# Performance work log

Measured on AMD Instinct MI355X. Metric: run time of the kernel, lower is better.

The kernel has to match this reference:

```python
import jax, jax.numpy as jnp
import numpy as np

N_NODES = 50000
N_EDGES = 640000
IN_CH = 128
OUT_CH = 128


def setup_inputs() -> dict:
    key = jax.random.key(0)
    k1, k2, k3, k4 = jax.random.split(key, 4)
    x = jax.random.normal(k1, (N_NODES, IN_CH), dtype=jnp.float32)
    edge_index = jax.random.randint(k2, (2, N_EDGES), 0, N_NODES, dtype=jnp.int32)
    # nn.Linear params: W [out, in], b [out]
    bound = 1.0 / np.sqrt(IN_CH)
    W = jax.random.uniform(k3, (OUT_CH, IN_CH), minval=-bound, maxval=bound, dtype=jnp.float32)
    b = jax.random.uniform(k4, (OUT_CH,), minval=-bound, maxval=bound, dtype=jnp.float32)
    return {"x": x, "edge_index": edge_index, "W": W, "b": b}


def reference(x, edge_index, W, b):
    row, col = edge_index[0], edge_index[1]
    num_nodes = x.shape[0]
    # degree of each destination node (clamped to >= 1)
    deg = jax.ops.segment_sum(jnp.ones(row.shape[0], dtype=x.dtype), row,
                              num_segments=num_nodes)
    deg = jnp.maximum(deg, 1.0)
    # gather neighbor features and scatter-add into destinations
    agg = jax.ops.segment_sum(x[col], row, num_segments=num_nodes)
    agg = agg / deg[:, None]
    # residual + linear
    return (x + agg) @ W.T + b
```

## Files before the change

kernel.cpp:

```cpp
#include <hip/hip_runtime.h>

#define N_NODES 50000
#define N_EDGES 640000
#define CH 128
#define NBINS 391
#define BINCAP 2048
#define CAPR 48
#define NTILES 3125
#define FILLB 157

typedef __bf16 bf16_t;
typedef bf16_t bf16x8 __attribute__((ext_vector_type(8)));
typedef float f32x4 __attribute__((ext_vector_type(4)));

__device__ __forceinline__ ushort f2bf(float f) {
  union { float f; unsigned u; } v; v.f = f;
  unsigned r = v.u + 0x7FFFu + ((v.u >> 16) & 1u);
  return (ushort)(r >> 16);
}
__device__ __forceinline__ float bflo(unsigned u) {
  union { unsigned u; float f; } v; v.u = u << 16; return v.f;
}
__device__ __forceinline__ float bfhi(unsigned u) {
  union { unsigned u; float f; } v; v.u = u & 0xFFFF0000u; return v.f;
}
__device__ __forceinline__ unsigned pack2(float lo, float hi) {
  return (unsigned)f2bf(lo) | ((unsigned)f2bf(hi) << 16);
}


__global__ __launch_bounds__(256) void fill_conv(const int* __restrict__ row,
                                                 const int* __restrict__ col,
                                                 int* __restrict__ bincur,
                                                 unsigned* __restrict__ binArr,
                                                 const float4* __restrict__ x4,
                                                 uint4* __restrict__ xb4,
                                                 const float4* __restrict__ W4,
                                                 uint4* __restrict__ Wb4) {
  int bid = blockIdx.x;
  int tid = threadIdx.x;
  if (bid < FILLB) {
    __shared__ int lh[NBINS];
    __shared__ int gb[NBINS];
    for (int i = tid; i < NBINS; i += 256) lh[i] = 0;
    __syncthreads();
    int base = bid * 4096 + tid * 16;
    bool act = base < N_EDGES;
    int rr[16], cc[16], bi[16], rk[16];
    if (act) {
#pragma unroll
      for (int u = 0; u < 4; ++u) {
        int4 r4 = *(const int4*)(row + base + u * 4);
        int4 c4 = *(const int4*)(col + base + u * 4);
        rr[u * 4 + 0] = r4.x; rr[u * 4 + 1] = r4.y; rr[u * 4 + 2] = r4.z; rr[u * 4 + 3] = r4.w;
        cc[u * 4 + 0] = c4.x; cc[u * 4 + 1] = c4.y; cc[u * 4 + 2] = c4.z; cc[u * 4 + 3] = c4.w;
      }
#pragma unroll
      for (int i = 0; i < 16; ++i) {
        bi[i] = rr[i] >> 7;
        rk[i] = atomicAdd(&lh[bi[i]], 1);
      }
    }
    __syncthreads();
    for (int i = tid; i < NBINS; i += 256) {
      int c = lh[i];
      gb[i] = c ? atomicAdd(&bincur[i], c) : 0;
    }
    __syncthreads();
    if (act) {
#pragma unroll
      for (int i = 0; i < 16; ++i) {
        int pos = gb[bi[i]] + rk[i];
        if (pos < BINCAP) {
          binArr[bi[i] * BINCAP + pos] =
              ((unsigned)(rr[i] & 127) << 16) | (unsigned)cc[i];
        }
      }
    }
  } else if (bid < FILLB + 3125) {
    int i = (bid - FILLB) * 256 + tid;
    float4 a = x4[i * 2], b = x4[i * 2 + 1];
    uint4 o;
    o.x = pack2(a.x, a.y); o.y = pack2(a.z, a.w);
    o.z = pack2(b.x, b.y); o.w = pack2(b.z, b.w);
    xb4[i] = o;
  } else {
    for (int i = tid; i < 2048; i += 256) {
      float4 c = W4[i * 2], d = W4[i * 2 + 1];
      uint4 w;
      w.x = pack2(c.x, c.y); w.y = pack2(c.z, c.w);
      w.z = pack2(d.x, d.y); w.w = pack2(d.z, d.w);
      Wb4[i] = w;
    }
  }
}

__global__ __launch_bounds__(128) void fused(const uint4* __restrict__ xb4,
                                             const int* __restrict__ bincnt,
                                             const uint4* __restrict__ binArr4,
                                             const uint4* __restrict__ Wb4,
                                             const float4* __restrict__ bias4,
                                             float4* __restrict__ out4) {
  __shared__ ushort hT[16 * CH];
  __shared__ ushort colL[16 * CAPR];
  __shared__ int rowcnt[16];
  int tid = threadIdx.x;
  int g = blockIdx.x;
  int m0 = g * 16;

  if (tid < 16) rowcnt[tid] = 0;
  __syncthreads();
  {
    int b = g >> 3;
    int sub = g & 7;
    int bc = bincnt[b]; bc = bc < BINCAP ? bc : BINCAP;
    const uint4* seg4 = binArr4 + b * (BINCAP / 4);
    for (int j = tid; j * 4 < bc; j += 128) {
      uint4 rv = seg4[j];
      int base = j * 4;
      unsigned recs[4] = {rv.x, rv.y, rv.z, rv.w};
#pragma unroll
      for (int i = 0; i < 4; ++i) {
        unsigned rec = recs[i];
        if (base + i < bc && (int)((rec >> 20) & 7) == sub) {
          int lr = (rec >> 16) & 15;
          int p = atomicAdd(&rowcnt[lr], 1);
          if (p < CAPR) colL[lr * CAPR + p] = (ushort)(rec & 0xFFFFu);
        }
      }
    }
  }
  __syncthreads();

  int wv = tid >> 6;
  int lane = tid & 63;
  int q = lane & 15;
  int grp = lane >> 4;
#pragma unroll
  for (int t = 0; t < 2; ++t) {
    int r = wv * 8 + t * 4 + grp;
    int node = m0 + r;
    int deg = rowcnt[r];
    int degc = deg < CAPR ? deg : CAPR;
    const ushort* arow = colL + r * CAPR;
    float acc[8] = {0.f, 0.f, 0.f, 0.f, 0.f, 0.f, 0.f, 0.f};
    int e = 0;
    for (; e + 3 < degc; e += 4) {
      uint2 ids = *(const uint2*)(arow + e);
      int n0 = ids.x & 0xFFFF, n1 = ids.x >> 16;
      int n2 = ids.y & 0xFFFF, n3 = ids.y >> 16;
      uint4 v0 = xb4[n0 * 16 + q];
      uint4 v1 = xb4[n1 * 16 + q];
      uint4 v2 = xb4[n2 * 16 + q];
      uint4 v3 = xb4[n3 * 16 + q];
      acc[0] += bflo(v0.x); acc[1] += bfhi(v0.x); acc[2] += bflo(v0.y); acc[3] += bfhi(v0.y);
      acc[4] += bflo(v0.z); acc[5] += bfhi(v0.z); acc[6] += bflo(v0.w); acc[7] += bfhi(v0.w);
      acc[0] += bflo(v1.x); acc[1] += bfhi(v1.x); acc[2] += bflo(v1.y); acc[3] += bfhi(v1.y);
      acc[4] += bflo(v1.z); acc[5] += bfhi(v1.z); acc[6] += bflo(v1.w); acc[7] += bfhi(v1.w);
      acc[0] += bflo(v2.x); acc[1] += bfhi(v2.x); acc[2] += bflo(v2.y); acc[3] += bfhi(v2.y);
      acc[4] += bflo(v2.z); acc[5] += bfhi(v2.z); acc[6] += bflo(v2.w); acc[7] += bfhi(v2.w);
      acc[0] += bflo(v3.x); acc[1] += bfhi(v3.x); acc[2] += bflo(v3.y); acc[3] += bfhi(v3.y);
      acc[4] += bflo(v3.z); acc[5] += bfhi(v3.z); acc[6] += bflo(v3.w); acc[7] += bfhi(v3.w);
    }
    for (; e < degc; ++e) {
      int nb = arow[e];
      uint4 v = xb4[nb * 16 + q];
      acc[0] += bflo(v.x); acc[1] += bfhi(v.x); acc[2] += bflo(v.y); acc[3] += bfhi(v.y);
      acc[4] += bflo(v.z); acc[5] += bfhi(v.z); acc[6] += bflo(v.w); acc[7] += bfhi(v.w);
    }
    float s = 1.0f / fmaxf((float)deg, 1.0f);
    uint4 xi = xb4[node * 16 + q];
    uint4 o;
    o.x = pack2(bflo(xi.x) + acc[0] * s, bfhi(xi.x) + acc[1] * s);
    o.y = pack2(bflo(xi.y) + acc[2] * s, bfhi(xi.y) + acc[3] * s);
    o.z = pack2(bflo(xi.z) + acc[4] * s, bfhi(xi.z) + acc[5] * s);
    o.w = pack2(bflo(xi.w) + acc[6] * s, bfhi(xi.w) + acc[7] * s);
    *(uint4*)&hT[r * CH + q * 8] = o;
  }
  __syncthreads();

  int qq = grp;
  const ushort* hrow = &hT[q * CH + qq * 8];
  bf16x8 hb0 = *(const bf16x8*)(hrow);
  bf16x8 hb1 = *(const bf16x8*)(hrow + 32);
  bf16x8 hb2 = *(const bf16x8*)(hrow + 64);
  bf16x8 hb3 = *(const bf16x8*)(hrow + 96);
  int m = m0 + q;
#pragma unroll
  for (int i = 0; i < 4; ++i) {
    int nt = wv * 4 + i;
    const uint4* wr = Wb4 + (nt * 16 + q) * 16 + qq;
    bf16x8 w0 = __builtin_bit_cast(bf16x8, wr[0]);
    bf16x8 w1 = __builtin_bit_cast(bf16x8, wr[4]);
    bf16x8 w2 = __builtin_bit_cast(bf16x8, wr[8]);
    bf16x8 w3 = __builtin_bit_cast(bf16x8, wr[12]);
    f32x4 acc = {0.f, 0.f, 0.f, 0.f};
    acc = __builtin_amdgcn_mfma_f32_16x16x32_bf16(w0, hb0, acc, 0, 0, 0);
    acc = __builtin_amdgcn_mfma_f32_16x16x32_bf16(w1, hb1, acc, 0, 0, 0);
    acc = __builtin_amdgcn_mfma_f32_16x16x32_bf16(w2, hb2, acc, 0, 0, 0);
    acc = __builtin_amdgcn_mfma_f32_16x16x32_bf16(w3, hb3, acc, 0, 0, 0);
    float4 bv = bias4[nt * 4 + qq];
    float4 o;
    o.x = acc[0] + bv.x;
    o.y = acc[1] + bv.y;
    o.z = acc[2] + bv.z;
    o.w = acc[3] + bv.w;
    out4[(size_t)m * 32 + nt * 4 + qq] = o;
  }
}

extern "C" void kernel_launch(void* const* d_in, const int* in_sizes, int n_in,
                              void* d_out, int out_size, void* d_ws, size_t ws_size,
                              hipStream_t stream) {
  const float* x  = (const float*)d_in[0];
  const int*   ei = (const int*)d_in[1];
  const float* W  = (const float*)d_in[2];
  const float* bb = (const float*)d_in[3];

  char* ws = (char*)d_ws;
  int*      bincur = (int*)ws;
  unsigned* binArr = (unsigned*)(ws + 2048);
  uint4*    Wb4    = (uint4*)(ws + 3205120);
  uint4*    xb4    = (uint4*)(ws + 3237888);

  hipMemsetAsync(bincur, 0, NBINS * sizeof(int), stream);
  fill_conv<<<FILLB + 3125 + 1, 256, 0, stream>>>(ei, ei + N_EDGES, bincur,
                                                  binArr, (const float4*)x, xb4,
                                                  (const float4*)W, Wb4);
  fused<<<NTILES, 128, 0, stream>>>(xb4, bincur, (const uint4*)binArr, Wb4,
                                    (const float4*)bb, (float4*)d_out);
}
```

Before: 129.3 us.

## Apply linear layer before aggregation and gather transformed features

Uses linearity to compute y = x·Wᵀ in the first kernel, alongside the edge binning, with W and x converted to bf16 on the fly. The second kernel then gathers bf16 rows of y, averages them, and adds the fp32 y row and bias, dropping its shared-memory staging and MFMA stage. In exchange, the first kernel now writes y in both fp32 and bf16, and the second kernel reads the fp32 copy back. That adds noticeable global memory traffic compared with writing a single bf16 copy of x.

```diff
diff --git a/kernel.cpp b/kernel.cpp
--- a/kernel.cpp
+++ b/kernel.cpp
@@ -6,8 +6,9 @@
 #define NBINS 391
 #define BINCAP 2048
 #define CAPR 48
+#define FILLB 157
+#define GEMMT 3125
 #define NTILES 3125
-#define FILLB 157
 
 typedef __bf16 bf16_t;
 typedef bf16_t bf16x8 __attribute__((ext_vector_type(8)));
@@ -27,16 +28,22 @@
 __device__ __forceinline__ unsigned pack2(float lo, float hi) {
   return (unsigned)f2bf(lo) | ((unsigned)f2bf(hi) << 16);
 }
-
-
-__global__ __launch_bounds__(256) void fill_conv(const int* __restrict__ row,
+__device__ __forceinline__ bf16x8 pack8(float4 a, float4 b) {
+  uint4 u;
+  u.x = pack2(a.x, a.y); u.y = pack2(a.z, a.w);
+  u.z = pack2(b.x, b.y); u.w = pack2(b.z, b.w);
+  return __builtin_bit_cast(bf16x8, u);
+}
+
+
+__global__ __launch_bounds__(256) void fill_gemm(const int* __restrict__ row,
                                                  const int* __restrict__ col,
                                                  int* __restrict__ bincur,
                                                  unsigned* __restrict__ binArr,
                                                  const float4* __restrict__ x4,
-                                                 uint4* __restrict__ xb4,
                                                  const float4* __restrict__ W4,
-                                                 uint4* __restrict__ Wb4) {
+                                                 float4* __restrict__ y4,
+                                                 ushort* __restrict__ yb) {
   int bid = blockIdx.x;
   int tid = threadIdx.x;
   if (bid < FILLB) {
@@ -77,31 +84,48 @@
         }
       }
     }
-  } else if (bid < FILLB + 3125) {
-    int i = (bid - FILLB) * 256 + tid;
-    float4 a = x4[i * 2], b = x4[i * 2 + 1];
-    uint4 o;
-    o.x = pack2(a.x, a.y); o.y = pack2(a.z, a.w);
-    o.z = pack2(b.x, b.y); o.w = pack2(b.z, b.w);
-    xb4[i] = o;
   } else {
-    for (int i = tid; i < 2048; i += 256) {
-      float4 c = W4[i * 2], d = W4[i * 2 + 1];
-      uint4 w;
-      w.x = pack2(c.x, c.y); w.y = pack2(c.z, c.w);
-      w.z = pack2(d.x, d.y); w.w = pack2(d.z, d.w);
-      Wb4[i] = w;
+    int g = bid - FILLB;
+    int m0 = g * 16;
+    int wv = tid >> 6;
+    int lane = tid & 63;
+    int q = lane & 15;
+    int qq = lane >> 4;
+    int m = m0 + q;
+    const float4* xr = x4 + (size_t)m * 32;
+    bf16x8 xb0 = pack8(xr[0 + 2 * qq], xr[1 + 2 * qq]);
+    bf16x8 xb1 = pack8(xr[8 + 2 * qq], xr[9 + 2 * qq]);
+    bf16x8 xb2 = pack8(xr[16 + 2 * qq], xr[17 + 2 * qq]);
+    bf16x8 xb3 = pack8(xr[24 + 2 * qq], xr[25 + 2 * qq]);
+#pragma unroll
+    for (int i = 0; i < 2; ++i) {
+      int nt = wv * 2 + i;
+      const float4* wr = W4 + (size_t)(nt * 16 + q) * 32;
+      bf16x8 w0 = pack8(wr[0 + 2 * qq], wr[1 + 2 * qq]);
+      bf16x8 w1 = pack8(wr[8 + 2 * qq], wr[9 + 2 * qq]);
+      bf16x8 w2 = pack8(wr[16 + 2 * qq], wr[17 + 2 * qq]);
+      bf16x8 w3 = pack8(wr[24 + 2 * qq], wr[25 + 2 * qq]);
+      f32x4 acc = {0.f, 0.f, 0.f, 0.f};
+      acc = __builtin_amdgcn_mfma_f32_16x16x32_bf16(w0, xb0, acc, 0, 0, 0);
+      acc = __builtin_amdgcn_mfma_f32_16x16x32_bf16(w1, xb1, acc, 0, 0, 0);
+      acc = __builtin_amdgcn_mfma_f32_16x16x32_bf16(w2, xb2, acc, 0, 0, 0);
+      acc = __builtin_amdgcn_mfma_f32_16x16x32_bf16(w3, xb3, acc, 0, 0, 0);
+      float4 o;
+      o.x = acc[0]; o.y = acc[1]; o.z = acc[2]; o.w = acc[3];
+      y4[(size_t)m * 32 + nt * 4 + qq] = o;
+      ushort4 u;
+      u.x = f2bf(o.x); u.y = f2bf(o.y); u.z = f2bf(o.z); u.w = f2bf(o.w);
+      *(ushort4*)(yb + (size_t)m * CH + nt * 16 + qq * 4) = u;
     }
   }
 }
 
-__global__ __launch_bounds__(128) void fused(const uint4* __restrict__ xb4,
-                                             const int* __restrict__ bincnt,
-                                             const uint4* __restrict__ binArr4,
-                                             const uint4* __restrict__ Wb4,
-                                             const float4* __restrict__ bias4,
-                                             float4* __restrict__ out4) {
-  __shared__ ushort hT[16 * CH];
+__global__ __launch_bounds__(128) void gather_out(const uint4* __restrict__ yb4,
+                                                  const int* __restrict__ bincnt,
+                                                  const uint4* __restrict__ binArr4,
+                                                  const float4* __restrict__ y4,
+                                                  const float4* __restrict__ bias4,
+                                                  float4* __restrict__ out4) {
   __shared__ ushort colL[16 * CAPR];
   __shared__ int rowcnt[16];
   int tid = threadIdx.x;
@@ -132,8 +156,8 @@
   }
   __syncthreads();
 
+  int lane = tid & 63;
   int wv = tid >> 6;
-  int lane = tid & 63;
   int q = lane & 15;
   int grp = lane >> 4;
 #pragma unroll
@@ -149,10 +173,10 @@
       uint2 ids = *(const uint2*)(arow + e);
       int n0 = ids.x & 0xFFFF, n1 = ids.x >> 16;
       int n2 = ids.y & 0xFFFF, n3 = ids.y >> 16;
-      uint4 v0 = xb4[n0 * 16 + q];
-      uint4 v1 = xb4[n1 * 16 + q];
-      uint4 v2 = xb4[n2 * 16 + q];
-      uint4 v3 = xb4[n3 * 16 + q];
+      uint4 v0 = yb4[n0 * 16 + q];
+      uint4 v1 = yb4[n1 * 16 + q];
+      uint4 v2 = yb4[n2 * 16 + q];
+      uint4 v3 = yb4[n3 * 16 + q];
       acc[0] += bflo(v0.x); acc[1] += bfhi(v0.x); acc[2] += bflo(v0.y); acc[3] += bfhi(v0.y);
       acc[4] += bflo(v0.z); acc[5] += bfhi(v0.z); acc[6] += bflo(v0.w); acc[7] += bfhi(v0.w);
       acc[0] += bflo(v1.x); acc[1] += bfhi(v1.x); acc[2] += bflo(v1.y); acc[3] += bfhi(v1.y);
@@ -164,48 +188,26 @@
     }
     for (; e < degc; ++e) {
       int nb = arow[e];
-      uint4 v = xb4[nb * 16 + q];
+      uint4 v = yb4[nb * 16 + q];
       acc[0] += bflo(v.x); acc[1] += bfhi(v.x); acc[2] += bflo(v.y); acc[3] += bfhi(v.y);
       acc[4] += bflo(v.z); acc[5] += bfhi(v.z); acc[6] += bflo(v.w); acc[7] += bfhi(v.w);
     }
     float s = 1.0f / fmaxf((float)deg, 1.0f);
-    uint4 xi = xb4[node * 16 + q];
-    uint4 o;
-    o.x = pack2(bflo(xi.x) + acc[0] * s, bfhi(xi.x) + acc[1] * s);
-    o.y = pack2(bflo(xi.y) + acc[2] * s, bfhi(xi.y) + acc[3] * s);
-    o.z = pack2(bflo(xi.z) + acc[4] * s, bfhi(xi.z) + acc[5] * s);
-    o.w = pack2(bflo(xi.w) + acc[6] * s, bfhi(xi.w) + acc[7] * s);
-    *(uint4*)&hT[r * CH + q * 8] = o;
-  }
-  __syncthreads();
-
-  int qq = grp;
-  const ushort* hrow = &hT[q * CH + qq * 8];
-  bf16x8 hb0 = *(const bf16x8*)(hrow);
-  bf16x8 hb1 = *(const bf16x8*)(hrow + 32);
-  bf16x8 hb2 = *(const bf16x8*)(hrow + 64);
-  bf16x8 hb3 = *(const bf16x8*)(hrow + 96);
-  int m = m0 + q;
-#pragma unroll
-  for (int i = 0; i < 4; ++i) {
-    int nt = wv * 4 + i;
-    const uint4* wr = Wb4 + (nt * 16 + q) * 16 + qq;
-    bf16x8 w0 = __builtin_bit_cast(bf16x8, wr[0]);
-    bf16x8 w1 = __builtin_bit_cast(bf16x8, wr[4]);
-    bf16x8 w2 = __builtin_bit_cast(bf16x8, wr[8]);
-    bf16x8 w3 = __builtin_bit_cast(bf16x8, wr[12]);
-    f32x4 acc = {0.f, 0.f, 0.f, 0.f};
-    acc = __builtin_amdgcn_mfma_f32_16x16x32_bf16(w0, hb0, acc, 0, 0, 0);
-    acc = __builtin_amdgcn_mfma_f32_16x16x32_bf16(w1, hb1, acc, 0, 0, 0);
-    acc = __builtin_amdgcn_mfma_f32_16x16x32_bf16(w2, hb2, acc, 0, 0, 0);
-    acc = __builtin_amdgcn_mfma_f32_16x16x32_bf16(w3, hb3, acc, 0, 0, 0);
-    float4 bv = bias4[nt * 4 + qq];
-    float4 o;
-    o.x = acc[0] + bv.x;
-    o.y = acc[1] + bv.y;
-    o.z = acc[2] + bv.z;
-    o.w = acc[3] + bv.w;
-    out4[(size_t)m * 32 + nt * 4 + qq] = o;
+    float4 ya = y4[(size_t)node * 32 + 2 * q];
+    float4 yb_ = y4[(size_t)node * 32 + 2 * q + 1];
+    float4 ba = bias4[2 * q];
+    float4 bb = bias4[2 * q + 1];
+    float4 o1, o2;
+    o1.x = ya.x + acc[0] * s + ba.x;
+    o1.y = ya.y + acc[1] * s + ba.y;
+    o1.z = ya.z + acc[2] * s + ba.z;
+    o1.w = ya.w + acc[3] * s + ba.w;
+    o2.x = yb_.x + acc[4] * s + bb.x;
+    o2.y = yb_.y + acc[5] * s + bb.y;
+    o2.z = yb_.z + acc[6] * s + bb.z;
+    o2.w = yb_.w + acc[7] * s + bb.w;
+    out4[(size_t)node * 32 + 2 * q] = o1;
+    out4[(size_t)node * 32 + 2 * q + 1] = o2;
   }
 }
 
@@ -220,13 +222,14 @@
   char* ws = (char*)d_ws;
   int*      bincur = (int*)ws;
   unsigned* binArr = (unsigned*)(ws + 2048);
-  uint4*    Wb4    = (uint4*)(ws + 3205120);
-  uint4*    xb4    = (uint4*)(ws + 3237888);
+  float4*   y4     = (float4*)(ws + 3205120);
+  ushort*   yb     = (ushort*)(ws + 28805120);
 
   hipMemsetAsync(bincur, 0, NBINS * sizeof(int), stream);
-  fill_conv<<<FILLB + 3125 + 1, 256, 0, stream>>>(ei, ei + N_EDGES, bincur,
-                                                  binArr, (const float4*)x, xb4,
-                                                  (const float4*)W, Wb4);
-  fused<<<NTILES, 128, 0, stream>>>(xb4, bincur, (const uint4*)binArr, Wb4,
-                                    (const float4*)bb, (float4*)d_out);
-}
+  fill_gemm<<<FILLB + GEMMT, 256, 0, stream>>>(ei, ei + N_EDGES, bincur, binArr,
+                                               (const float4*)x, (const float4*)W,
+                                               y4, yb);
+  gather_out<<<NTILES, 128, 0, stream>>>((const uint4*)yb, bincur,
+                                         (const uint4*)binArr, (const float4*)y4,
+                                         (const float4*)bb, (float4*)d_out);
+}
```

After: 149.7 us. 1.16x slower.
